# Optimization experiments

Measured on AMD Instinct MI355X. Metric: run time of the kernel, lower is better.

## Reference

```python
import jax, jax.numpy as jnp
import numpy as np

IN_FEATURES = 4096
OUT_FEATURES = 11008
BLOCK_SIZE = 64
BITS = 4
RANGE_MAX = 2 ** (BITS - 1) - 1  # 7


def setup_inputs() -> dict:
    key = jax.random.key(0)
    k1, k2, k3, k4 = jax.random.split(key, 4)
    n_blocks = OUT_FEATURES * IN_FEATURES // BLOCK_SIZE
    x = jax.random.normal(k1, (4, 2048, IN_FEATURES), dtype=jnp.float32)
    # int4 codes in [-7, 7]; stored signed int. Use randint in [-7, 8).
    weight_quant = jax.random.randint(k2, (n_blocks, BLOCK_SIZE), -RANGE_MAX, RANGE_MAX + 1, dtype=jnp.int32)
    weight_absmax = jax.random.uniform(k3, (n_blocks, 1), dtype=jnp.float32, minval=1e-5, maxval=1.0)
    bias = jax.random.normal(k4, (OUT_FEATURES,), dtype=jnp.float32)
    return {"x": x, "weight_quant": weight_quant, "weight_absmax": weight_absmax, "bias": bias}


def reference(x, weight_quant, weight_absmax, bias):
    # Blockwise dequant: q/range_max * absmax per block, reshape to (out, in). padding=0.
    w = (weight_quant.astype(jnp.float32) / RANGE_MAX) * weight_absmax  # [n_blocks, block]
    w = w.reshape(OUT_FEATURES, IN_FEATURES)
    # F.linear: y = x @ W^T + b
    return jnp.einsum('bsi,oi->bso', x, w) + bias
```

## Files before the change

### kernel.cpp

```cpp
#include <hip/hip_runtime.h>


#define K_DIM 4096
#define N_DIM 11008
#define M_DIM 8192
#define NT_K 64
#define AB_OFF 98304
#define TILE_BYTES 2097152

typedef _Float16 f16;
typedef _Float16 f16x8 __attribute__((ext_vector_type(8)));
typedef float f32x16 __attribute__((ext_vector_type(16)));
typedef float fv4 __attribute__((ext_vector_type(4)));
typedef int iv4 __attribute__((ext_vector_type(4)));

__device__ __forceinline__ void gload16(const void* g, void* lds) {
  __builtin_amdgcn_global_load_lds(
      (__attribute__((address_space(1))) void*)g,
      (__attribute__((address_space(3))) void*)lds,
      16, 0, 0);
}

__global__ __launch_bounds__(256) void prep_kernel(const float* __restrict__ x,
                                                   f16* __restrict__ xo, int n16x,
                                                   const int* __restrict__ q,
                                                   const float* __restrict__ amax,
                                                   f16* __restrict__ wo, int n16w) {
  int i = blockIdx.x * blockDim.x + threadIdx.x;
  if (i < n16x) {
    const int lam = i & 63;
    const int F = (i >> 6) & 15;
    const int kk = (i >> 10) & 1;
    const int t = (i >> 11) & 63;
    const int mt = i >> 17;
    const int row = mt * 256 + ((F >> 1) << 5) + (lam & 31);
    const int kc = t * 64 + (kk << 5) + ((F & 1) << 4) + ((lam >> 5) << 3);
    const fv4* src = (const fv4*)(x + (size_t)row * K_DIM + kc);
    fv4 a = __builtin_nontemporal_load(src);
    fv4 b = __builtin_nontemporal_load(src + 1);
    f16x8 o;
    o[0] = (f16)a.x; o[1] = (f16)a.y; o[2] = (f16)a.z; o[3] = (f16)a.w;
    o[4] = (f16)b.x; o[5] = (f16)b.y; o[6] = (f16)b.z; o[7] = (f16)b.w;
    *(f16x8*)(xo + (size_t)i * 8) = o;
  } else {
    int j = i - n16x;
    if (j >= n16w) return;
    const int lam = j & 63;
    const int F = (j >> 6) & 15;
    const int kk = (j >> 10) & 1;
    const int t = (j >> 11) & 63;
    const int nt = j >> 17;
    const int row = nt * 256 + ((F >> 1) << 5) + (lam & 31);
    const int kc = t * 64 + (kk << 5) + ((F & 1) << 4) + ((lam >> 5) << 3);
    const size_t base = (size_t)row * K_DIM + kc;
    const iv4* src = (const iv4*)(q + base);
    iv4 a = __builtin_nontemporal_load(src);
    iv4 b = __builtin_nontemporal_load(src + 1);
    float s = amax[base >> 6] * (1.0f / 7.0f);
    f16x8 o;
    o[0] = (f16)((float)a.x * s); o[1] = (f16)((float)a.y * s);
    o[2] = (f16)((float)a.z * s); o[3] = (f16)((float)a.w * s);
    o[4] = (f16)((float)b.x * s); o[5] = (f16)((float)b.y * s);
    o[6] = (f16)((float)b.z * s); o[7] = (f16)((float)b.w * s);
    *(f16x8*)(wo + (size_t)j * 8) = o;
  }
}

__device__ __forceinline__ void read_frags(const char* ldsc, int abase, int bbase, int kk, int ks,
                                           int aF0, int bF0, int l16,
                                           f16x8 (&af)[4], f16x8 (&bf)[2]) {
#pragma unroll
  for (int mf = 0; mf < 4; ++mf)
    af[mf] = *(const f16x8*)(ldsc + abase + kk * 16384 + aF0 + (((mf << 1) | ks) << 10) + l16);
#pragma unroll
  for (int nf = 0; nf < 2; ++nf)
    bf[nf] = *(const f16x8*)(ldsc + bbase + kk * 16384 + bF0 + (((nf << 1) | ks) << 10) + l16);
}

__device__ __forceinline__ void mfma8(const f16x8 (&af)[4], const f16x8 (&bf)[2],
                                      f32x16 (&acc)[4][2]) {
  __builtin_amdgcn_s_setprio(1);
#pragma unroll
  for (int mf = 0; mf < 4; ++mf)
#pragma unroll
    for (int nf = 0; nf < 2; ++nf)
      acc[mf][nf] = __builtin_amdgcn_mfma_f32_32x32x16_f16(af[mf], bf[nf], acc[mf][nf], 0, 0, 0);
  __builtin_amdgcn_s_setprio(0);
}

__global__ __launch_bounds__(512, 2) void gemm_f16_bt(const f16* __restrict__ A,
                                                      const f16* __restrict__ B,
                                                      const float* __restrict__ bias,
                                                      float* __restrict__ C) {
  __shared__ __align__(16) char lds[163840];

  const int tid = threadIdx.x;
  const int w = tid >> 6;
  const int l = tid & 63;
  const int wr = w >> 2;
  const int wc = w & 3;

  const int wg = blockIdx.x;
  const int swz = (wg & 7) * 172 + (wg >> 3);
  const int mt = swz / 43;
  const int nt = swz % 43;
  const int m0 = mt * 256;
  const int n0 = nt * 256;

  const char* Abase = (const char*)A + (size_t)mt * TILE_BYTES + (w << 10) + (l << 4);
  const char* Bbase = (const char*)B + (size_t)nt * TILE_BYTES + (w << 10) + (l << 4);

  char* ldsc = (char*)lds;

#define STAGE_A(dst_off, koff)                 \
  {                                            \
    char* d_ = ldsc + (dst_off) + (w << 10);   \
    gload16(Abase + (koff), d_);               \
    gload16(Abase + (koff) + 8192, d_ + 8192); \
  }
#define STAGE_B(dst_off, koff)                 \
  {                                            \
    char* d_ = ldsc + (dst_off) + (w << 10);   \
    gload16(Bbase + (koff), d_);               \
    gload16(Bbase + (koff) + 8192, d_ + 8192); \
  }

  f32x16 acc[4][2];
#pragma unroll
  for (int i = 0; i < 4; ++i)
#pragma unroll
    for (int j = 0; j < 2; ++j) acc[i][j] = (f32x16)0.f;

  const int l16 = l << 4;
  const int aF0 = wr << 13;
  const int bF0 = wc << 12;

  STAGE_A(0, 0);
  STAGE_A(16384, 16384);
  STAGE_B(AB_OFF, 0);
  STAGE_B(AB_OFF + 16384, 16384);
  STAGE_A(32768, 32768);
  STAGE_A(32768 + 16384, 32768 + 16384);
  STAGE_B(AB_OFF + 32768, 32768);
  asm volatile("s_waitcnt vmcnt(6)" ::: "memory");
  __builtin_amdgcn_s_barrier();

  int ap = 0;
  int ap2 = 65536;

  f16x8 afe[4], bfe[2];
  f16x8 afo[4], bfo[2];

  read_frags(ldsc, 0, AB_OFF, 0, 0, aF0, bF0, l16, afe, bfe);

  for (int t = 0; t < NT_K; ++t) {
    const int p = t & 1;
    const int pn = p ^ 1;
    const int Bb = AB_OFF + p * 32768;
    const int Bn = AB_OFF + pn * 32768;
    const int t1 = (t + 1 < NT_K) ? (t + 1) : (NT_K - 1);
    const int t2 = (t + 2 < NT_K) ? (t + 2) : (NT_K - 1);
    const int k1 = t1 * 32768;
    const int k2 = t2 * 32768;

    read_frags(ldsc, ap, Bb, 0, 1, aF0, bF0, l16, afo, bfo);
    STAGE_B(Bn + 16384, k1 + 16384);
    mfma8(afe, bfe, acc);

    read_frags(ldsc, ap, Bb, 1, 0, aF0, bF0, l16, afe, bfe);
    STAGE_A(ap2, k2);
    mfma8(afo, bfo, acc);
    __builtin_amdgcn_s_barrier();

    read_frags(ldsc, ap, Bb, 1, 1, aF0, bF0, l16, afo, bfo);
    STAGE_A(ap2 + 16384, k2 + 16384);
    mfma8(afe, bfe, acc);

    STAGE_B(Bb, k2);
    mfma8(afo, bfo, acc);
    asm volatile("s_waitcnt vmcnt(6)" ::: "memory");
    __builtin_amdgcn_s_barrier();

    const int apN = (ap + 32768 == AB_OFF) ? 0 : ap + 32768;
    read_frags(ldsc, apN, Bn, 0, 0, aF0, bF0, l16, afe, bfe);
    ap = apN;
    ap2 = (ap2 + 32768 == AB_OFF) ? 0 : ap2 + 32768;
  }

  const int l31 = l & 31;
  const int rbase = 4 * (l >> 5);
  float bv[2];
#pragma unroll
  for (int nf = 0; nf < 2; ++nf) bv[nf] = bias[n0 + wc * 64 + nf * 32 + l31];
#pragma unroll
  for (int mf = 0; mf < 4; ++mf) {
#pragma unroll
    for (int nf = 0; nf < 2; ++nf) {
      const size_t col = n0 + wc * 64 + nf * 32 + l31;
#pragma unroll
      for (int qd = 0; qd < 4; ++qd) {
#pragma unroll
        for (int j = 0; j < 4; ++j) {
          const int row = m0 + wr * 128 + mf * 32 + rbase + 8 * qd + j;
          __builtin_nontemporal_store(acc[mf][nf][qd * 4 + j] + bv[nf],
                                      &C[(size_t)row * N_DIM + col]);
        }
      }
    }
  }
#undef STAGE_A
#undef STAGE_B
}

extern "C" void kernel_launch(void* const* d_in, const int* in_sizes, int n_in,
                              void* d_out, int out_size, void* d_ws, size_t ws_size,
                              hipStream_t stream) {
  const float* x = (const float*)d_in[0];
  const int* wq = (const int*)d_in[1];
  const float* amax = (const float*)d_in[2];
  const float* bias = (const float*)d_in[3];
  float* out = (float*)d_out;

  f16* Xh = (f16*)d_ws;
  f16* Wh = (f16*)((char*)d_ws + (size_t)M_DIM * K_DIM * 2);

  {
    int n16x = M_DIM * K_DIM / 8;
    int n16w = N_DIM * K_DIM / 8;
    int nthr = n16x + n16w;
    prep_kernel<<<(nthr + 255) / 256, 256, 0, stream>>>(x, Xh, n16x, wq, amax, Wh, n16w);
  }
  {
    dim3 grid((M_DIM / 256) * (N_DIM / 256));
    gemm_f16_bt<<<grid, 512, 0, stream>>>(Xh, Wh, bias, out);
  }
}
```

Before: 874.8 us.

## Restructure GEMM main loop into quadrant-wise 8-phase schedule with extra barriers

The K-tile loop changes from four fragment-pair MFMA groups with double-buffered register fragments to four output quadrants (A half × B column). Each quadrant loads its full K-slice of fragments, then runs 8 MFMAs behind explicit lgkmcnt waits, sched_barriers and extra workgroup barriers. The aim is to reuse A/B fragments in registers across quadrants and interleave the two co-resident workgroups in ping-pong fashion. The cost is more barriers per iteration, and fragment loads are no longer prefetched across iterations, so LDS latency may be exposed.

```diff
diff --git a/kernel.cpp b/kernel.cpp
--- a/kernel.cpp
+++ b/kernel.cpp
@@ -66,28 +66,6 @@
   }
 }
 
-__device__ __forceinline__ void read_frags(const char* ldsc, int abase, int bbase, int kk, int ks,
-                                           int aF0, int bF0, int l16,
-                                           f16x8 (&af)[4], f16x8 (&bf)[2]) {
-#pragma unroll
-  for (int mf = 0; mf < 4; ++mf)
-    af[mf] = *(const f16x8*)(ldsc + abase + kk * 16384 + aF0 + (((mf << 1) | ks) << 10) + l16);
-#pragma unroll
-  for (int nf = 0; nf < 2; ++nf)
-    bf[nf] = *(const f16x8*)(ldsc + bbase + kk * 16384 + bF0 + (((nf << 1) | ks) << 10) + l16);
-}
-
-__device__ __forceinline__ void mfma8(const f16x8 (&af)[4], const f16x8 (&bf)[2],
-                                      f32x16 (&acc)[4][2]) {
-  __builtin_amdgcn_s_setprio(1);
-#pragma unroll
-  for (int mf = 0; mf < 4; ++mf)
-#pragma unroll
-    for (int nf = 0; nf < 2; ++nf)
-      acc[mf][nf] = __builtin_amdgcn_mfma_f32_32x32x16_f16(af[mf], bf[nf], acc[mf][nf], 0, 0, 0);
-  __builtin_amdgcn_s_setprio(0);
-}
-
 __global__ __launch_bounds__(512, 2) void gemm_f16_bt(const f16* __restrict__ A,
                                                       const f16* __restrict__ B,
                                                       const float* __restrict__ bias,
@@ -109,8 +87,8 @@
 
   const char* Abase = (const char*)A + (size_t)mt * TILE_BYTES + (w << 10) + (l << 4);
   const char* Bbase = (const char*)B + (size_t)nt * TILE_BYTES + (w << 10) + (l << 4);
-
   char* ldsc = (char*)lds;
+  const int l16 = l << 4;
 
 #define STAGE_A(dst_off, koff)                 \
   {                                            \
@@ -124,16 +102,37 @@
     gload16(Bbase + (koff), d_);               \
     gload16(Bbase + (koff) + 8192, d_ + 8192); \
   }
+#define READ_A(mh)                                                            \
+  {                                                                           \
+    _Pragma("unroll") for (int m = 0; m < 2; ++m)                             \
+    _Pragma("unroll") for (int ks = 0; ks < 4; ++ks) {                        \
+      const int rowblk = (wr << 2) + ((mh) << 1) + m;                         \
+      a8[m * 4 + ks] = *(const f16x8*)(ldsc + ap + ((ks >> 1) << 14) +        \
+                                       (((rowblk << 1) | (ks & 1)) << 10) + l16); \
+    }                                                                         \
+  }
+#define READ_B(nf)                                                            \
+  {                                                                           \
+    const int colblk = (wc << 1) + (nf);                                      \
+    _Pragma("unroll") for (int ks = 0; ks < 4; ++ks)                          \
+      b8[(nf)][ks] = *(const f16x8*)(ldsc + Bb + ((ks >> 1) << 14) +          \
+                                     (((colblk << 1) | (ks & 1)) << 10) + l16); \
+  }
+#define MFMA_Q(mh, nf)                                                        \
+  {                                                                           \
+    __builtin_amdgcn_s_setprio(1);                                            \
+    _Pragma("unroll") for (int ks = 0; ks < 4; ++ks)                          \
+    _Pragma("unroll") for (int m = 0; m < 2; ++m)                             \
+      acc[(mh) * 2 + m][(nf)] = __builtin_amdgcn_mfma_f32_32x32x16_f16(       \
+          a8[m * 4 + ks], b8[(nf)][ks], acc[(mh) * 2 + m][(nf)], 0, 0, 0);    \
+    __builtin_amdgcn_s_setprio(0);                                            \
+  }
 
   f32x16 acc[4][2];
 #pragma unroll
   for (int i = 0; i < 4; ++i)
 #pragma unroll
     for (int j = 0; j < 2; ++j) acc[i][j] = (f32x16)0.f;
-
-  const int l16 = l << 4;
-  const int aF0 = wr << 13;
-  const int bF0 = wc << 12;
 
   STAGE_A(0, 0);
   STAGE_A(16384, 16384);
@@ -148,10 +147,8 @@
   int ap = 0;
   int ap2 = 65536;
 
-  f16x8 afe[4], bfe[2];
-  f16x8 afo[4], bfo[2];
-
-  read_frags(ldsc, 0, AB_OFF, 0, 0, aF0, bF0, l16, afe, bfe);
+  f16x8 a8[8];
+  f16x8 b8[2][4];
 
   for (int t = 0; t < NT_K; ++t) {
     const int p = t & 1;
@@ -163,28 +160,40 @@
     const int k1 = t1 * 32768;
     const int k2 = t2 * 32768;
 
-    read_frags(ldsc, ap, Bb, 0, 1, aF0, bF0, l16, afo, bfo);
+    READ_A(0);
+    READ_B(0);
     STAGE_B(Bn + 16384, k1 + 16384);
-    mfma8(afe, bfe, acc);
-
-    read_frags(ldsc, ap, Bb, 1, 0, aF0, bF0, l16, afe, bfe);
+    asm volatile("s_waitcnt lgkmcnt(8)" ::: "memory");
+    __builtin_amdgcn_s_barrier();
+    asm volatile("s_waitcnt lgkmcnt(0)" ::: "memory");
+    __builtin_amdgcn_sched_barrier(0);
+    MFMA_Q(0, 0);
+    __builtin_amdgcn_s_barrier();
+
+    READ_B(1);
     STAGE_A(ap2, k2);
-    mfma8(afo, bfo, acc);
-    __builtin_amdgcn_s_barrier();
-
-    read_frags(ldsc, ap, Bb, 1, 1, aF0, bF0, l16, afo, bfo);
+    __builtin_amdgcn_s_barrier();
+    asm volatile("s_waitcnt lgkmcnt(0)" ::: "memory");
+    __builtin_amdgcn_sched_barrier(0);
+    MFMA_Q(0, 1);
+    __builtin_amdgcn_s_barrier();
+
+    READ_A(1);
     STAGE_A(ap2 + 16384, k2 + 16384);
-    mfma8(afe, bfe, acc);
+    __builtin_amdgcn_s_barrier();
+    asm volatile("s_waitcnt lgkmcnt(0)" ::: "memory");
+    __builtin_amdgcn_sched_barrier(0);
+    MFMA_Q(1, 1);
+    __builtin_amdgcn_s_barrier();
 
     STAGE_B(Bb, k2);
-    mfma8(afo, bfo, acc);
+    __builtin_amdgcn_s_barrier();
+    MFMA_Q(1, 0);
     asm volatile("s_waitcnt vmcnt(6)" ::: "memory");
     __builtin_amdgcn_s_barrier();
 
-    const int apN = (ap + 32768 == AB_OFF) ? 0 : ap + 32768;
-    read_frags(ldsc, apN, Bn, 0, 0, aF0, bF0, l16, afe, bfe);
-    ap = apN;
-    ap2 = (ap2 + 32768 == AB_OFF) ? 0 : ap2 + 32768;
+    ap += 32768;  if (ap == AB_OFF) ap = 0;
+    ap2 += 32768; if (ap2 == AB_OFF) ap2 = 0;
   }
 
   const int l31 = l & 31;
@@ -210,6 +219,9 @@
   }
 #undef STAGE_A
 #undef STAGE_B
+#undef READ_A
+#undef READ_B
+#undef MFMA_Q
 }
 
 extern "C" void kernel_launch(void* const* d_in, const int* in_sizes, int n_in,
```

Measured after the change: 889.4 us. No clear change (+1.7%).
